# Kernel tuning notes

Hardware: AMD Instinct MI355X
Metric: run time of the kernel (lower is better)

## Reference

```python
import jax, jax.numpy as jnp
from jax import lax
import numpy as np

B, CIN, H, W = 64, 3, 256, 256
K, D = 512, 4
EPS = 1e-5

def conv(x, w, s, p):
    return lax.conv_general_dilated(x, w, (s, s), [(p, p), (p, p)],
                                    dimension_numbers=('NCHW', 'OIHW', 'NCHW'))

def convT(x, w, s, p):
    # w in torch ConvTranspose2d layout (Cin, Cout, kh, kw)
    wt = jnp.flip(w, (2, 3)).transpose(1, 0, 2, 3)
    kh, kw = w.shape[2], w.shape[3]
    pad = [(kh - 1 - p, kh - 1 - p), (kw - 1 - p, kw - 1 - p)]
    return lax.conv_general_dilated(x, wt, (1, 1), pad, lhs_dilation=(s, s),
                                    dimension_numbers=('NCHW', 'OIHW', 'NCHW'))

def bn(x, g, b):
    # training-mode BatchNorm2d: batch stats over (N,H,W), biased variance
    m = jnp.mean(x, (0, 2, 3), keepdims=True)
    v = jnp.var(x, (0, 2, 3), keepdims=True)
    return g[None, :, None, None] * (x - m) * lax.rsqrt(v + EPS) + b[None, :, None, None]

def setup_inputs() -> dict:
    key = jax.random.key(0)
    ks = jax.random.split(key, 8)
    rn = lambda k, s: jax.random.normal(k, s, jnp.float32) * 0.05
    return {
        'x': jax.random.uniform(ks[0], (B, CIN, H, W), jnp.float32),
        'enc_w1': rn(ks[1], (8, CIN, 5, 5)),
        'enc_g1': jnp.ones(8, jnp.float32), 'enc_b1': jnp.zeros(8, jnp.float32),
        'enc_w2': rn(ks[2], (16, 8, 3, 3)),
        'enc_g2': jnp.ones(16, jnp.float32), 'enc_b2': jnp.zeros(16, jnp.float32),
        'enc_w3': rn(ks[3], (D, 16, 3, 3)),
        'enc_g3': jnp.ones(D, jnp.float32), 'enc_b3': jnp.zeros(D, jnp.float32),
        'emb': jax.random.uniform(ks[4], (K, D), jnp.float32, -1.0 / K, 1.0 / K),
        'dec_w1': rn(ks[5], (D, 16, 3, 3)),
        'dec_g1': jnp.ones(16, jnp.float32), 'dec_b1': jnp.zeros(16, jnp.float32),
        'dec_w2': rn(ks[6], (16, 8, 3, 3)),
        'dec_g2': jnp.ones(8, jnp.float32), 'dec_b2': jnp.zeros(8, jnp.float32),
        'dec_w3': rn(ks[7], (8, CIN, 2, 2)),
        'dec_bias3': jnp.zeros(CIN, jnp.float32),
    }

def reference(x, enc_w1, enc_g1, enc_b1, enc_w2, enc_g2, enc_b2,
              enc_w3, enc_g3, enc_b3, emb,
              dec_w1, dec_g1, dec_b1, dec_w2, dec_g2, dec_b2,
              dec_w3, dec_bias3):
    # encoder: 256 -> 127 -> 64 -> 32
    h1 = jax.nn.relu(bn(conv(x, enc_w1, 2, 1), enc_g1, enc_b1))
    h2 = jax.nn.relu(bn(conv(h1, enc_w2, 2, 1), enc_g2, enc_b2))
    latents = jax.nn.relu(bn(conv(h2, enc_w3, 2, 1), enc_g3, enc_b3))  # [B, D, h, w]
    Bq, Dq, h, w = latents.shape
    z = latents.transpose(0, 2, 3, 1).reshape(-1, Dq)  # [N, D] tokens
    # VQ: squared L2 distances (expanded form, as in 'efficient' path), argmin, gather
    dist = (jnp.sum(z * z, 1, keepdims=True)
            - 2.0 * (z @ emb.T)
            + jnp.sum(emb * emb, 1)[None, :])  # [N, K]
    closest = jnp.argmin(dist, axis=-1)
    codes = emb[closest]  # same math as one-hot @ emb
    codebook_loss = jnp.mean((codes - lax.stop_gradient(z)) ** 2)
    commitment_loss = jnp.mean((lax.stop_gradient(codes) - z) ** 2)
    codes = z + lax.stop_gradient(codes - z)  # straight-through
    quantized = codes.reshape(Bq, h, w, Dq).transpose(0, 3, 1, 2)  # [B, D, h, w]
    # decoder: 32 -> 65 -> 129 -> 256
    g1 = jax.nn.relu(bn(convT(quantized, dec_w1, 2, 0), dec_g1, dec_b1))
    g2 = jax.nn.relu(bn(convT(g1, dec_w2, 2, 1), dec_g2, dec_b2))
    decoded = jax.nn.sigmoid(convT(g2, dec_w3, 2, 1) + dec_bias3[None, :, None, None])
    return (latents, quantized, decoded, codebook_loss, commitment_loss)
```

## Files before the change

kernel.cpp:

```cpp
#include <hip/hip_runtime.h>
#include <hip/hip_bf16.h>
#include <math.h>


#define EPSV 1e-5f

template<int CIN, int COUT, int KH, int KW, int S, int P,
         int IH, int IW, int OH, int OW, bool FUSE>
__global__ __launch_bounds__(256)
void conv_all(const float* __restrict__ in, const float* __restrict__ w,
              const float* __restrict__ ssin, float* __restrict__ out,
              float* __restrict__ psum, float* __restrict__ psq) {
    __shared__ float wl[COUT * CIN * KH * KW];
    __shared__ float ssl[2 * CIN];
    __shared__ float redbuf[4 * 2 * COUT];
    const int n = blockIdx.z;
    for (int i = threadIdx.x; i < COUT * CIN * KH * KW; i += 256) wl[i] = w[i];
    if constexpr (FUSE) {
        for (int i = threadIdx.x; i < 2 * CIN; i += 256) ssl[i] = ssin[i];
    }
    __syncthreads();

    const int p = blockIdx.x * 256 + threadIdx.x;
    const int oy = p / OW, ox = p % OW;
    float acc[COUT];
    #pragma unroll
    for (int co = 0; co < COUT; ++co) acc[co] = 0.f;

    if (p < OH * OW) {
        const int iy0 = oy * S - P, ix0 = ox * S - P;
        const float* inb = in + (size_t)n * CIN * IH * IW;
        #pragma unroll
        for (int ci = 0; ci < CIN; ++ci) {
            #pragma unroll
            for (int kh = 0; kh < KH; ++kh) {
                const int iy = iy0 + kh;
                if ((unsigned)iy < (unsigned)IH) {
                    #pragma unroll
                    for (int kw = 0; kw < KW; ++kw) {
                        const int ix = ix0 + kw;
                        if ((unsigned)ix < (unsigned)IW) {
                            float v = inb[(ci * IH + iy) * IW + ix];
                            if constexpr (FUSE)
                                v = fmaxf(v * ssl[2 * ci] + ssl[2 * ci + 1], 0.f);
                            #pragma unroll
                            for (int co = 0; co < COUT; ++co)
                                acc[co] += v * wl[((co * CIN + ci) * KH + kh) * KW + kw];
                        }
                    }
                }
            }
        }
        #pragma unroll
        for (int co = 0; co < COUT; ++co)
            out[(((size_t)n * COUT + co) * OH + oy) * OW + ox] = acc[co];
    }

    const int lane = threadIdx.x & 63, wid = threadIdx.x >> 6;
    #pragma unroll
    for (int co = 0; co < COUT; ++co) {
        float s = acc[co], q = acc[co] * acc[co];
        #pragma unroll
        for (int o = 32; o > 0; o >>= 1) {
            s += __shfl_down(s, o, 64);
            q += __shfl_down(q, o, 64);
        }
        if (lane == 0) {
            redbuf[wid * 2 * COUT + 2 * co]     = s;
            redbuf[wid * 2 * COUT + 2 * co + 1] = q;
        }
    }
    __syncthreads();
    if (threadIdx.x < 2 * COUT) {
        const float v = redbuf[threadIdx.x] + redbuf[2 * COUT + threadIdx.x]
                      + redbuf[4 * COUT + threadIdx.x] + redbuf[6 * COUT + threadIdx.x];
        const int co = threadIdx.x >> 1;
        const int bid = blockIdx.z * gridDim.x + blockIdx.x;
        const int NB  = gridDim.x * gridDim.z;
        if (threadIdx.x & 1) psq[co * NB + bid] = v;
        else                 psum[co * NB + bid] = v;
    }
}

template<int CIN, int COUT, int KH, int KW, int P,
         int IH, int IW, int OH, int OW, bool FUSE>
__global__ __launch_bounds__(256)
void convT_all(const float* __restrict__ in, const float* __restrict__ w,
               const float* __restrict__ ssin, float* __restrict__ out,
               float* __restrict__ psum, float* __restrict__ psq) {
    __shared__ float wl[CIN * COUT * KH * KW];
    __shared__ float ssl[2 * CIN];
    __shared__ float redbuf[4 * 2 * COUT];
    const int n = blockIdx.z;
    for (int i = threadIdx.x; i < CIN * COUT * KH * KW; i += 256) wl[i] = w[i];
    if constexpr (FUSE) {
        for (int i = threadIdx.x; i < 2 * CIN; i += 256) ssl[i] = ssin[i];
    }
    __syncthreads();

    const int p = blockIdx.x * 256 + threadIdx.x;
    const int oy = p / OW, ox = p % OW;
    float acc[COUT];
    #pragma unroll
    for (int co = 0; co < COUT; ++co) acc[co] = 0.f;

    if (p < OH * OW) {
        const float* inb = in + (size_t)n * CIN * IH * IW;
        #pragma unroll
        for (int kh = 0; kh < KH; ++kh) {
            const int t = oy + P - kh;
            const int iy = t >> 1;
            if (t >= 0 && (t & 1) == 0 && iy < IH) {
                #pragma unroll
                for (int kw = 0; kw < KW; ++kw) {
                    const int u = ox + P - kw;
                    const int ix = u >> 1;
                    if (u >= 0 && (u & 1) == 0 && ix < IW) {
                        #pragma unroll
                        for (int ci = 0; ci < CIN; ++ci) {
                            float v = inb[(ci * IH + iy) * IW + ix];
                            if constexpr (FUSE)
                                v = fmaxf(v * ssl[2 * ci] + ssl[2 * ci + 1], 0.f);
                            #pragma unroll
                            for (int co = 0; co < COUT; ++co)
                                acc[co] += v * wl[((ci * COUT + co) * KH + kh) * KW + kw];
                        }
                    }
                }
            }
        }
        #pragma unroll
        for (int co = 0; co < COUT; ++co)
            out[(((size_t)n * COUT + co) * OH + oy) * OW + ox] = acc[co];
    }

    const int lane = threadIdx.x & 63, wid = threadIdx.x >> 6;
    #pragma unroll
    for (int co = 0; co < COUT; ++co) {
        float s = acc[co], q = acc[co] * acc[co];
        #pragma unroll
        for (int o = 32; o > 0; o >>= 1) {
            s += __shfl_down(s, o, 64);
            q += __shfl_down(q, o, 64);
        }
        if (lane == 0) {
            redbuf[wid * 2 * COUT + 2 * co]     = s;
            redbuf[wid * 2 * COUT + 2 * co + 1] = q;
        }
    }
    __syncthreads();
    if (threadIdx.x < 2 * COUT) {
        const float v = redbuf[threadIdx.x] + redbuf[2 * COUT + threadIdx.x]
                      + redbuf[4 * COUT + threadIdx.x] + redbuf[6 * COUT + threadIdx.x];
        const int co = threadIdx.x >> 1;
        const int bid = blockIdx.z * gridDim.x + blockIdx.x;
        const int NB  = gridDim.x * gridDim.z;
        if (threadIdx.x & 1) psq[co * NB + bid] = v;
        else                 psum[co * NB + bid] = v;
    }
}

template<int C>
__global__ __launch_bounds__(64)
void red_final_k(const float* __restrict__ psum, const float* __restrict__ psq,
                 const float* __restrict__ g, const float* __restrict__ b,
                 float* __restrict__ ss, float inv_count, int NB) {
    const int c = blockIdx.x;
    float s = 0.f, q = 0.f;
    for (int i = threadIdx.x; i < NB; i += 64) { s += psum[c * NB + i]; q += psq[c * NB + i]; }
    #pragma unroll
    for (int o = 32; o > 0; o >>= 1) {
        s += __shfl_down(s, o, 64);
        q += __shfl_down(q, o, 64);
    }
    if (threadIdx.x == 0) {
        const float mean = s * inv_count;
        const float var  = q * inv_count - mean * mean;
        const float rstd = 1.f / sqrtf(var + EPSV);
        const float sc   = g[c] * rstd;
        ss[2 * c]     = sc;
        ss[2 * c + 1] = b[c] - mean * sc;
    }
}

__global__ __launch_bounds__(256)
void vq_k(const float* __restrict__ raw, const float* __restrict__ ss,
          const float* __restrict__ emb, float* __restrict__ out_lat,
          float* __restrict__ out_q, float* __restrict__ lossp) {
    __shared__ float e[512 * 4];
    __shared__ float ee[512];
    __shared__ float ssl[8];
    __shared__ float redbuf[4];
    for (int i = threadIdx.x; i < 512 * 4; i += 256) e[i] = emb[i];
    if (threadIdx.x < 8) ssl[threadIdx.x] = ss[threadIdx.x];
    __syncthreads();
    for (int k = threadIdx.x; k < 512; k += 256) {
        float s = 0.f;
        #pragma unroll
        for (int d = 0; d < 4; ++d) { const float v = e[k * 4 + d]; s += v * v; }
        ee[k] = s;
    }
    __syncthreads();

    const int t = blockIdx.x * 256 + threadIdx.x;
    const int b = t >> 10, p = t & 1023;
    const float* rb = raw + ((size_t)b * 4) * 1024 + p;
    const float z0 = fmaxf(rb[0]    * ssl[0] + ssl[1], 0.f);
    const float z1 = fmaxf(rb[1024] * ssl[2] + ssl[3], 0.f);
    const float z2 = fmaxf(rb[2048] * ssl[4] + ssl[5], 0.f);
    const float z3 = fmaxf(rb[3072] * ssl[6] + ssl[7], 0.f);
    float* lb = out_lat + ((size_t)b * 4) * 1024 + p;
    lb[0] = z0; lb[1024] = z1; lb[2048] = z2; lb[3072] = z3;

    const float zz = z0 * z0 + z1 * z1 + z2 * z2 + z3 * z3;
    int best = 0;
    float bd = INFINITY;
    #pragma unroll 8
    for (int k = 0; k < 512; ++k) {
        const float dot = z0 * e[k * 4] + z1 * e[k * 4 + 1] + z2 * e[k * 4 + 2] + z3 * e[k * 4 + 3];
        const float d = zz - 2.f * dot + ee[k];
        if (d < bd) { bd = d; best = k; }
    }
    const float q0 = e[best * 4], q1 = e[best * 4 + 1], q2 = e[best * 4 + 2], q3 = e[best * 4 + 3];
    float* qb = out_q + ((size_t)b * 4) * 1024 + p;
    qb[0] = q0; qb[1024] = q1; qb[2048] = q2; qb[3072] = q3;

    float ssd = (q0 - z0) * (q0 - z0) + (q1 - z1) * (q1 - z1)
              + (q2 - z2) * (q2 - z2) + (q3 - z3) * (q3 - z3);
    #pragma unroll
    for (int o = 32; o > 0; o >>= 1) ssd += __shfl_down(ssd, o, 64);
    const int lane = threadIdx.x & 63, wid = threadIdx.x >> 6;
    if (lane == 0) redbuf[wid] = ssd;
    __syncthreads();
    if (threadIdx.x == 0)
        lossp[blockIdx.x] = redbuf[0] + redbuf[1] + redbuf[2] + redbuf[3];
}

__global__ __launch_bounds__(256)
void loss_final_k(const float* __restrict__ partial, float* __restrict__ out_cb,
                  float* __restrict__ out_cm) {
    __shared__ float redbuf[4];
    float s = partial[threadIdx.x];
    #pragma unroll
    for (int o = 32; o > 0; o >>= 1) s += __shfl_down(s, o, 64);
    const int lane = threadIdx.x & 63, wid = threadIdx.x >> 6;
    if (lane == 0) redbuf[wid] = s;
    __syncthreads();
    if (threadIdx.x == 0) {
        const float L = (redbuf[0] + redbuf[1] + redbuf[2] + redbuf[3]) * (1.f / 262144.f);
        *out_cb = L;
        *out_cm = L;
    }
}

__global__ __launch_bounds__(256)
void convt3_k(const float* __restrict__ in, const float* __restrict__ w,
              const float* __restrict__ ss, const float* __restrict__ bias,
              float* __restrict__ out) {
    __shared__ float wl[8 * 3 * 4];
    __shared__ float ssl[16];
    __shared__ float bl[3];
    if (threadIdx.x < 96) wl[threadIdx.x] = w[threadIdx.x];
    if (threadIdx.x < 16) ssl[threadIdx.x] = ss[threadIdx.x];
    if (threadIdx.x < 3)  bl[threadIdx.x] = bias[threadIdx.x];
    __syncthreads();

    const int n = blockIdx.z;
    const int p = blockIdx.x * 256 + threadIdx.x;
    const int oy = p >> 8, ox = p & 255;
    const int kh = 1 - (oy & 1), kw = 1 - (ox & 1);
    const int iy = (oy + 1 - kh) >> 1, ix = (ox + 1 - kw) >> 1;
    const float* inb = in + (size_t)n * 8 * 129 * 129;

    float a0 = bl[0], a1 = bl[1], a2 = bl[2];
    const int wo = kh * 2 + kw;
    #pragma unroll
    for (int ci = 0; ci < 8; ++ci) {
        float v = inb[(ci * 129 + iy) * 129 + ix];
        v = fmaxf(v * ssl[2 * ci] + ssl[2 * ci + 1], 0.f);
        a0 += v * wl[(ci * 3 + 0) * 4 + wo];
        a1 += v * wl[(ci * 3 + 1) * 4 + wo];
        a2 += v * wl[(ci * 3 + 2) * 4 + wo];
    }
    a0 = 1.f / (1.f + expf(-a0));
    a1 = 1.f / (1.f + expf(-a1));
    a2 = 1.f / (1.f + expf(-a2));
    float* ob = out + ((size_t)n * 3 * 65536) + (size_t)oy * 256 + ox;
    ob[0] = a0; ob[65536] = a1; ob[131072] = a2;
}

extern "C" void kernel_launch(void* const* d_in, const int* in_sizes, int n_in,
                              void* d_out, int out_size, void* d_ws, size_t ws_size,
                              hipStream_t stream) {
    const float* x      = (const float*)d_in[0];
    const float* ew1    = (const float*)d_in[1];
    const float* eg1    = (const float*)d_in[2];
    const float* eb1    = (const float*)d_in[3];
    const float* ew2    = (const float*)d_in[4];
    const float* eg2    = (const float*)d_in[5];
    const float* eb2    = (const float*)d_in[6];
    const float* ew3    = (const float*)d_in[7];
    const float* eg3    = (const float*)d_in[8];
    const float* eb3    = (const float*)d_in[9];
    const float* emb    = (const float*)d_in[10];
    const float* dw1    = (const float*)d_in[11];
    const float* dg1    = (const float*)d_in[12];
    const float* db1    = (const float*)d_in[13];
    const float* dw2    = (const float*)d_in[14];
    const float* dg2    = (const float*)d_in[15];
    const float* db2    = (const float*)d_in[16];
    const float* dw3    = (const float*)d_in[17];
    const float* dbias3 = (const float*)d_in[18];

    float* out_lat = (float*)d_out;
    float* out_q   = out_lat + 262144;
    float* out_dec = out_q + 262144;
    float* out_cb  = (float*)d_out + 13107200;
    float* out_cm  = out_cb + 1;

    float* bufA  = (float*)d_ws;
    float* bufB  = bufA + 8520768;
    float* bufC  = bufB + 4326400;
    float* psum  = bufC + 262144;
    float* psq   = psum + 33792;
    float* ssb   = psq + 33792;
    float* lossp = ssb + 32;

    const int T = 256;

    conv_all<3, 8, 5, 5, 2, 1, 256, 256, 127, 127, false>
        <<<dim3(64, 1, 64), T, 0, stream>>>(x, ew1, nullptr, bufA, psum, psq);
    red_final_k<8><<<8, 64, 0, stream>>>(psum, psq, eg1, eb1, ssb,
                                         1.f / (64.f * 16129.f), 64 * 64);

    conv_all<8, 16, 3, 3, 2, 1, 127, 127, 64, 64, true>
        <<<dim3(16, 1, 64), T, 0, stream>>>(bufA, ew2, ssb, bufB, psum, psq);
    red_final_k<16><<<16, 64, 0, stream>>>(psum, psq, eg2, eb2, ssb,
                                           1.f / (64.f * 4096.f), 16 * 64);

    conv_all<16, 4, 3, 3, 2, 1, 64, 64, 32, 32, true>
        <<<dim3(4, 1, 64), T, 0, stream>>>(bufB, ew3, ssb, bufC, psum, psq);
    red_final_k<4><<<4, 64, 0, stream>>>(psum, psq, eg3, eb3, ssb,
                                         1.f / (64.f * 1024.f), 4 * 64);

    vq_k<<<256, T, 0, stream>>>(bufC, ssb, emb, out_lat, out_q, lossp);
    loss_final_k<<<1, T, 0, stream>>>(lossp, out_cb, out_cm);

    convT_all<4, 16, 3, 3, 0, 32, 32, 65, 65, false>
        <<<dim3(17, 1, 64), T, 0, stream>>>(out_q, dw1, nullptr, bufB, psum, psq);
    red_final_k<16><<<16, 64, 0, stream>>>(psum, psq, dg1, db1, ssb,
                                           1.f / (64.f * 4225.f), 17 * 64);

    convT_all<16, 8, 3, 3, 1, 65, 65, 129, 129, true>
        <<<dim3(66, 1, 64), T, 0, stream>>>(bufB, dw2, ssb, bufA, psum, psq);
    red_final_k<8><<<8, 64, 0, stream>>>(psum, psq, dg2, db2, ssb,
                                         1.f / (64.f * 16641.f), 66 * 64);

    convt3_k<<<dim3(256, 1, 64), T, 0, stream>>>(bufA, dw3, ssb, dbias3, out_dec);
}
```

Measured before the change: 504.8 us.

## Replace generic conv kernels with specialized per-layer tiled and parity-split kernels

Replaces the generic templated conv and transposed-conv kernels with a hand-specialized kernel per layer. The first conv stages an input tile in shared memory and computes several outputs per thread. The transposed convs are split by output-row parity so that only the valid taps are evaluated instead of branching on stride residues. The last decoder layer computes 2x2 outputs per thread and writes them as float2 with fast exp. The goals are more register reuse of weights, fewer wasted taps and better coalescing, at the cost of much more layer-specific code and index logic that must be checked for correctness.

```diff
diff --git a/kernel.cpp b/kernel.cpp
--- a/kernel.cpp
+++ b/kernel.cpp
@@ -5,158 +5,31 @@
 
 #define EPSV 1e-5f
 
-template<int CIN, int COUT, int KH, int KW, int S, int P,
-         int IH, int IW, int OH, int OW, bool FUSE>
-__global__ __launch_bounds__(256)
-void conv_all(const float* __restrict__ in, const float* __restrict__ w,
-              const float* __restrict__ ssin, float* __restrict__ out,
-              float* __restrict__ psum, float* __restrict__ psq) {
-    __shared__ float wl[COUT * CIN * KH * KW];
-    __shared__ float ssl[2 * CIN];
-    __shared__ float redbuf[4 * 2 * COUT];
-    const int n = blockIdx.z;
-    for (int i = threadIdx.x; i < COUT * CIN * KH * KW; i += 256) wl[i] = w[i];
-    if constexpr (FUSE) {
-        for (int i = threadIdx.x; i < 2 * CIN; i += 256) ssl[i] = ssin[i];
-    }
-    __syncthreads();
-
-    const int p = blockIdx.x * 256 + threadIdx.x;
-    const int oy = p / OW, ox = p % OW;
-    float acc[COUT];
-    #pragma unroll
-    for (int co = 0; co < COUT; ++co) acc[co] = 0.f;
-
-    if (p < OH * OW) {
-        const int iy0 = oy * S - P, ix0 = ox * S - P;
-        const float* inb = in + (size_t)n * CIN * IH * IW;
-        #pragma unroll
-        for (int ci = 0; ci < CIN; ++ci) {
-            #pragma unroll
-            for (int kh = 0; kh < KH; ++kh) {
-                const int iy = iy0 + kh;
-                if ((unsigned)iy < (unsigned)IH) {
-                    #pragma unroll
-                    for (int kw = 0; kw < KW; ++kw) {
-                        const int ix = ix0 + kw;
-                        if ((unsigned)ix < (unsigned)IW) {
-                            float v = inb[(ci * IH + iy) * IW + ix];
-                            if constexpr (FUSE)
-                                v = fmaxf(v * ssl[2 * ci] + ssl[2 * ci + 1], 0.f);
-                            #pragma unroll
-                            for (int co = 0; co < COUT; ++co)
-                                acc[co] += v * wl[((co * CIN + ci) * KH + kh) * KW + kw];
-                        }
-                    }
-                }
-            }
-        }
-        #pragma unroll
-        for (int co = 0; co < COUT; ++co)
-            out[(((size_t)n * COUT + co) * OH + oy) * OW + ox] = acc[co];
-    }
-
-    const int lane = threadIdx.x & 63, wid = threadIdx.x >> 6;
+template<int COUT, int NW>
+__device__ __forceinline__ void stats_write(float (&s)[COUT], float (&q)[COUT],
+    float* __restrict__ psum, float* __restrict__ psq, int bid, int NB,
+    float* redbuf, int tid) {
+    const int lane = tid & 63, wid = tid >> 6;
     #pragma unroll
     for (int co = 0; co < COUT; ++co) {
-        float s = acc[co], q = acc[co] * acc[co];
+        float ss = s[co], qq = q[co];
         #pragma unroll
         for (int o = 32; o > 0; o >>= 1) {
-            s += __shfl_down(s, o, 64);
-            q += __shfl_down(q, o, 64);
+            ss += __shfl_down(ss, o, 64);
+            qq += __shfl_down(qq, o, 64);
         }
         if (lane == 0) {
-            redbuf[wid * 2 * COUT + 2 * co]     = s;
-            redbuf[wid * 2 * COUT + 2 * co + 1] = q;
-        }
-    }
-    __syncthreads();
-    if (threadIdx.x < 2 * COUT) {
-        const float v = redbuf[threadIdx.x] + redbuf[2 * COUT + threadIdx.x]
-                      + redbuf[4 * COUT + threadIdx.x] + redbuf[6 * COUT + threadIdx.x];
-        const int co = threadIdx.x >> 1;
-        const int bid = blockIdx.z * gridDim.x + blockIdx.x;
-        const int NB  = gridDim.x * gridDim.z;
-        if (threadIdx.x & 1) psq[co * NB + bid] = v;
-        else                 psum[co * NB + bid] = v;
-    }
-}
-
-template<int CIN, int COUT, int KH, int KW, int P,
-         int IH, int IW, int OH, int OW, bool FUSE>
-__global__ __launch_bounds__(256)
-void convT_all(const float* __restrict__ in, const float* __restrict__ w,
-               const float* __restrict__ ssin, float* __restrict__ out,
-               float* __restrict__ psum, float* __restrict__ psq) {
-    __shared__ float wl[CIN * COUT * KH * KW];
-    __shared__ float ssl[2 * CIN];
-    __shared__ float redbuf[4 * 2 * COUT];
-    const int n = blockIdx.z;
-    for (int i = threadIdx.x; i < CIN * COUT * KH * KW; i += 256) wl[i] = w[i];
-    if constexpr (FUSE) {
-        for (int i = threadIdx.x; i < 2 * CIN; i += 256) ssl[i] = ssin[i];
-    }
-    __syncthreads();
-
-    const int p = blockIdx.x * 256 + threadIdx.x;
-    const int oy = p / OW, ox = p % OW;
-    float acc[COUT];
-    #pragma unroll
-    for (int co = 0; co < COUT; ++co) acc[co] = 0.f;
-
-    if (p < OH * OW) {
-        const float* inb = in + (size_t)n * CIN * IH * IW;
-        #pragma unroll
-        for (int kh = 0; kh < KH; ++kh) {
-            const int t = oy + P - kh;
-            const int iy = t >> 1;
-            if (t >= 0 && (t & 1) == 0 && iy < IH) {
-                #pragma unroll
-                for (int kw = 0; kw < KW; ++kw) {
-                    const int u = ox + P - kw;
-                    const int ix = u >> 1;
-                    if (u >= 0 && (u & 1) == 0 && ix < IW) {
-                        #pragma unroll
-                        for (int ci = 0; ci < CIN; ++ci) {
-                            float v = inb[(ci * IH + iy) * IW + ix];
-                            if constexpr (FUSE)
-                                v = fmaxf(v * ssl[2 * ci] + ssl[2 * ci + 1], 0.f);
-                            #pragma unroll
-                            for (int co = 0; co < COUT; ++co)
-                                acc[co] += v * wl[((ci * COUT + co) * KH + kh) * KW + kw];
-                        }
-                    }
-                }
-            }
-        }
-        #pragma unroll
-        for (int co = 0; co < COUT; ++co)
-            out[(((size_t)n * COUT + co) * OH + oy) * OW + ox] = acc[co];
-    }
-
-    const int lane = threadIdx.x & 63, wid = threadIdx.x >> 6;
-    #pragma unroll
-    for (int co = 0; co < COUT; ++co) {
-        float s = acc[co], q = acc[co] * acc[co];
-        #pragma unroll
-        for (int o = 32; o > 0; o >>= 1) {
-            s += __shfl_down(s, o, 64);
-            q += __shfl_down(q, o, 64);
-        }
-        if (lane == 0) {
-            redbuf[wid * 2 * COUT + 2 * co]     = s;
-            redbuf[wid * 2 * COUT + 2 * co + 1] = q;
-        }
-    }
-    __syncthreads();
-    if (threadIdx.x < 2 * COUT) {
-        const float v = redbuf[threadIdx.x] + redbuf[2 * COUT + threadIdx.x]
-                      + redbuf[4 * COUT + threadIdx.x] + redbuf[6 * COUT + threadIdx.x];
-        const int co = threadIdx.x >> 1;
-        const int bid = blockIdx.z * gridDim.x + blockIdx.x;
-        const int NB  = gridDim.x * gridDim.z;
-        if (threadIdx.x & 1) psq[co * NB + bid] = v;
-        else                 psum[co * NB + bid] = v;
+            redbuf[wid * 2 * COUT + 2 * co]     = ss;
+            redbuf[wid * 2 * COUT + 2 * co + 1] = qq;
+        }
+    }
+    __syncthreads();
+    if (tid < 2 * COUT) {
+        float v = 0.f;
+        #pragma unroll
+        for (int w = 0; w < NW; ++w) v += redbuf[w * 2 * COUT + tid];
+        if (tid & 1) psq [(tid >> 1) * NB + bid] = v;
+        else         psum[(tid >> 1) * NB + bid] = v;
     }
 }
 
@@ -181,6 +54,208 @@
         ss[2 * c]     = sc;
         ss[2 * c + 1] = b[c] - mean * sc;
     }
+}
+
+__global__ __launch_bounds__(128)
+void conv1_k(const float* __restrict__ in, const float* __restrict__ w,
+             float* __restrict__ out, float* __restrict__ psum,
+             float* __restrict__ psq) {
+    __shared__ float tile[3 * 11 * 264];
+    __shared__ float wl[600];
+    __shared__ float redbuf[2 * 2 * 8];
+    const int tid = threadIdx.x;
+    const int by = blockIdx.y, n = blockIdx.z;
+
+    for (int i = tid; i < 600; i += 128) {
+        const int co = i & 7, rest = i >> 3;
+        wl[i] = w[co * 75 + rest];
+    }
+    const int iy_org = 8 * by - 1;
+    const float* inb = in + (size_t)n * 3 * 256 * 256;
+    for (int i = tid; i < 3 * 11 * 264; i += 128) {
+        const int c = i % 264, rc = i / 264, r = rc % 11, ci = rc / 11;
+        const int gy = iy_org + r, gx = c - 1;
+        float v = 0.f;
+        if (c < 258 && (unsigned)gy < 256u && (unsigned)gx < 256u)
+            v = inb[(ci * 256 + gy) * 256 + gx];
+        tile[(ci * 11 + r) * 264 + c] = v;
+    }
+    __syncthreads();
+
+    const int ty = tid >> 5, tx = tid & 31;
+    const int oy = 4 * by + ty;
+    float acc[4][8];
+    #pragma unroll
+    for (int p = 0; p < 4; ++p)
+        #pragma unroll
+        for (int co = 0; co < 8; ++co) acc[p][co] = 0.f;
+
+    #pragma unroll
+    for (int ci = 0; ci < 3; ++ci) {
+        #pragma unroll
+        for (int kh = 0; kh < 5; ++kh) {
+            const float* trow = &tile[(ci * 11 + 2 * ty + kh) * 264];
+            #pragma unroll
+            for (int kw = 0; kw < 5; ++kw) {
+                float wv[8];
+                #pragma unroll
+                for (int co = 0; co < 8; ++co)
+                    wv[co] = wl[((ci * 5 + kh) * 5 + kw) * 8 + co];
+                #pragma unroll
+                for (int p = 0; p < 4; ++p) {
+                    const float v = trow[2 * (tx + 32 * p) + kw];
+                    #pragma unroll
+                    for (int co = 0; co < 8; ++co) acc[p][co] = fmaf(v, wv[co], acc[p][co]);
+                }
+            }
+        }
+    }
+    if (oy >= 127) {
+        #pragma unroll
+        for (int p = 0; p < 4; ++p)
+            #pragma unroll
+            for (int co = 0; co < 8; ++co) acc[p][co] = 0.f;
+    }
+    #pragma unroll
+    for (int p = 0; p < 4; ++p)
+        if (tx + 32 * p >= 127) {
+            #pragma unroll
+            for (int co = 0; co < 8; ++co) acc[p][co] = 0.f;
+        }
+    if (oy < 127) {
+        #pragma unroll
+        for (int p = 0; p < 4; ++p) {
+            const int ox = tx + 32 * p;
+            if (ox < 127) {
+                #pragma unroll
+                for (int co = 0; co < 8; ++co)
+                    out[(((size_t)n * 8 + co) * 127 + oy) * 127 + ox] = acc[p][co];
+            }
+        }
+    }
+    float s[8], q[8];
+    #pragma unroll
+    for (int co = 0; co < 8; ++co) {
+        s[co] = acc[0][co] + acc[1][co] + acc[2][co] + acc[3][co];
+        q[co] = acc[0][co] * acc[0][co] + acc[1][co] * acc[1][co]
+              + acc[2][co] * acc[2][co] + acc[3][co] * acc[3][co];
+    }
+    stats_write<8, 2>(s, q, psum, psq, n * 32 + by, 2048, redbuf, tid);
+}
+
+__global__ __launch_bounds__(256)
+void conv2_k(const float* __restrict__ in, const float* __restrict__ w,
+             const float* __restrict__ ssin, float* __restrict__ out,
+             float* __restrict__ psum, float* __restrict__ psq) {
+    __shared__ float wl[8 * 9 * 16];
+    __shared__ float ssl[16];
+    __shared__ float redbuf[4 * 2 * 16];
+    const int tid = threadIdx.x;
+    const int by = blockIdx.y, n = blockIdx.z;
+    for (int i = tid; i < 1152; i += 256) {
+        const int co = i & 15, rest = i >> 4;
+        wl[i] = w[co * 72 + rest];
+    }
+    if (tid < 16) ssl[tid] = ssin[tid];
+    __syncthreads();
+
+    const int ty = tid >> 5, tx = tid & 31;
+    const int oy = 8 * by + ty;
+    const float* inb = in + (size_t)n * 8 * 127 * 127;
+    float acc[2][16];
+    #pragma unroll
+    for (int p = 0; p < 2; ++p)
+        #pragma unroll
+        for (int co = 0; co < 16; ++co) acc[p][co] = 0.f;
+
+    #pragma unroll
+    for (int ci = 0; ci < 8; ++ci) {
+        const float sc = ssl[2 * ci], sh = ssl[2 * ci + 1];
+        #pragma unroll
+        for (int kh = 0; kh < 3; ++kh) {
+            const int iy = 2 * oy - 1 + kh;
+            const bool vy = (unsigned)iy < 127u;
+            #pragma unroll
+            for (int kw = 0; kw < 3; ++kw) {
+                float wv[16];
+                #pragma unroll
+                for (int co = 0; co < 16; ++co)
+                    wv[co] = wl[(ci * 9 + kh * 3 + kw) * 16 + co];
+                #pragma unroll
+                for (int p = 0; p < 2; ++p) {
+                    const int ox = tx + 32 * p;
+                    const int ix = 2 * ox - 1 + kw;
+                    float v = 0.f;
+                    if (vy && (unsigned)ix < 127u)
+                        v = fmaxf(inb[(ci * 127 + iy) * 127 + ix] * sc + sh, 0.f);
+                    #pragma unroll
+                    for (int co = 0; co < 16; ++co) acc[p][co] = fmaf(v, wv[co], acc[p][co]);
+                }
+            }
+        }
+    }
+    #pragma unroll
+    for (int p = 0; p < 2; ++p) {
+        const int ox = tx + 32 * p;
+        #pragma unroll
+        for (int co = 0; co < 16; ++co)
+            out[(((size_t)n * 16 + co) * 64 + oy) * 64 + ox] = acc[p][co];
+    }
+    float s[16], q[16];
+    #pragma unroll
+    for (int co = 0; co < 16; ++co) {
+        s[co] = acc[0][co] + acc[1][co];
+        q[co] = acc[0][co] * acc[0][co] + acc[1][co] * acc[1][co];
+    }
+    stats_write<16, 4>(s, q, psum, psq, n * 8 + by, 512, redbuf, tid);
+}
+
+__global__ __launch_bounds__(256)
+void conv3_k(const float* __restrict__ in, const float* __restrict__ w,
+             const float* __restrict__ ssin, float* __restrict__ out,
+             float* __restrict__ psum, float* __restrict__ psq) {
+    __shared__ float wl[16 * 9 * 4];
+    __shared__ float ssl[32];
+    __shared__ float redbuf[4 * 2 * 4];
+    const int tid = threadIdx.x;
+    const int bx = blockIdx.x, n = blockIdx.z;
+    for (int i = tid; i < 576; i += 256) {
+        const int co = i & 3, rest = i >> 2;
+        wl[i] = w[co * 144 + rest];
+    }
+    if (tid < 32) ssl[tid] = ssin[tid];
+    __syncthreads();
+
+    const int p = bx * 256 + tid;
+    const int oy = p >> 5, ox = p & 31;
+    const float* inb = in + (size_t)n * 16 * 64 * 64;
+    float acc[4] = {0.f, 0.f, 0.f, 0.f};
+    #pragma unroll
+    for (int ci = 0; ci < 16; ++ci) {
+        const float sc = ssl[2 * ci], sh = ssl[2 * ci + 1];
+        #pragma unroll
+        for (int kh = 0; kh < 3; ++kh) {
+            const int iy = 2 * oy - 1 + kh;
+            const bool vy = (unsigned)iy < 64u;
+            #pragma unroll
+            for (int kw = 0; kw < 3; ++kw) {
+                const int ix = 2 * ox - 1 + kw;
+                float v = 0.f;
+                if (vy && (unsigned)ix < 64u)
+                    v = fmaxf(inb[(ci * 64 + iy) * 64 + ix] * sc + sh, 0.f);
+                #pragma unroll
+                for (int co = 0; co < 4; ++co)
+                    acc[co] = fmaf(v, wl[(ci * 9 + kh * 3 + kw) * 4 + co], acc[co]);
+            }
+        }
+    }
+    #pragma unroll
+    for (int co = 0; co < 4; ++co)
+        out[((size_t)n * 4 + co) * 1024 + p] = acc[co];
+    float s[4], q[4];
+    #pragma unroll
+    for (int co = 0; co < 4; ++co) { s[co] = acc[co]; q[co] = acc[co] * acc[co]; }
+    stats_write<4, 4>(s, q, psum, psq, n * 4 + bx, 256, redbuf, tid);
 }
 
 __global__ __launch_bounds__(256)
@@ -254,39 +329,185 @@
 }
 
 __global__ __launch_bounds__(256)
-void convt3_k(const float* __restrict__ in, const float* __restrict__ w,
-              const float* __restrict__ ss, const float* __restrict__ bias,
-              float* __restrict__ out) {
-    __shared__ float wl[8 * 3 * 4];
+void dect1_k(const float* __restrict__ in, const float* __restrict__ w,
+             float* __restrict__ out, float* __restrict__ psum,
+             float* __restrict__ psq) {
+    __shared__ float wl[4 * 9 * 16];
+    __shared__ float redbuf[4 * 2 * 16];
+    const int tid = threadIdx.x;
+    const int cy = blockIdx.y, n = blockIdx.z;
+    for (int i = tid; i < 576; i += 256) {
+        const int co = i & 15, rest = i >> 4;
+        const int ci = rest / 9, k = rest % 9;
+        wl[i] = w[(ci * 16 + co) * 9 + k];
+    }
+    __syncthreads();
+
+    const int Ry = 33 - cy;
+    const int p = blockIdx.x * 256 + tid;
+    const bool active = p < Ry * 33;
+    const int ry = p / 33, rx = p % 33;
+    const int oy = 2 * ry + cy;
+    float acc_e[16], acc_o[16];
+    #pragma unroll
+    for (int co = 0; co < 16; ++co) { acc_e[co] = 0.f; acc_o[co] = 0.f; }
+
+    if (active) {
+        const float* inb = in + (size_t)n * 4 * 1024;
+        auto tap = [&](int kh, int iy, bool vy) {
+            #pragma unroll
+            for (int ci = 0; ci < 4; ++ci) {
+                const float* r = inb + (ci * 32 + iy) * 32;
+                const float vL = (vy && rx >= 1) ? r[rx - 1] : 0.f;
+                const float vR = (vy && rx < 32) ? r[rx]     : 0.f;
+                const float* wp = &wl[(ci * 9 + kh * 3) * 16];
+                #pragma unroll
+                for (int co = 0; co < 16; ++co) {
+                    acc_e[co] = fmaf(vR, wp[co], fmaf(vL, wp[32 + co], acc_e[co]));
+                    acc_o[co] = fmaf(vR, wp[16 + co], acc_o[co]);
+                }
+            }
+        };
+        if (cy == 0) { tap(0, ry, ry < 32); tap(2, ry - 1, ry >= 1); }
+        else         { tap(1, ry, true); }
+
+        #pragma unroll
+        for (int co = 0; co < 16; ++co) {
+            float* o = out + (((size_t)n * 16 + co) * 65 + oy) * 65 + 2 * rx;
+            o[0] = acc_e[co];
+            if (rx < 32) o[1] = acc_o[co];
+        }
+    }
+    float s[16], q[16];
+    #pragma unroll
+    for (int co = 0; co < 16; ++co) {
+        s[co] = acc_e[co] + acc_o[co];
+        q[co] = acc_e[co] * acc_e[co] + acc_o[co] * acc_o[co];
+    }
+    stats_write<16, 4>(s, q, psum, psq, (n * 2 + cy) * 5 + blockIdx.x, 640, redbuf, tid);
+}
+
+__global__ __launch_bounds__(256)
+void dect2_k(const float* __restrict__ in, const float* __restrict__ w,
+             const float* __restrict__ ssin, float* __restrict__ out,
+             float* __restrict__ psum, float* __restrict__ psq) {
+    __shared__ float wl[16 * 9 * 8];
+    __shared__ float ssl[32];
+    __shared__ float redbuf[4 * 2 * 8];
+    const int tid = threadIdx.x;
+    const int cy = blockIdx.y, n = blockIdx.z;
+    for (int i = tid; i < 1152; i += 256) {
+        const int co = i & 7, rest = i >> 3;
+        const int ci = rest / 9, k = rest % 9;
+        wl[i] = w[(ci * 8 + co) * 9 + k];
+    }
+    if (tid < 32) ssl[tid] = ssin[tid];
+    __syncthreads();
+
+    const int Ry = 65 - cy;
+    const int p = blockIdx.x * 256 + tid;
+    const bool active = p < Ry * 65;
+    const int ry = p / 65, rx = p % 65;
+    const int oy = 2 * ry + cy;
+    float acc_e[8], acc_o[8];
+    #pragma unroll
+    for (int co = 0; co < 8; ++co) { acc_e[co] = 0.f; acc_o[co] = 0.f; }
+
+    if (active) {
+        const float* inb = in + (size_t)n * 16 * 65 * 65;
+        auto tap = [&](int kh, int iy) {
+            #pragma unroll
+            for (int ci = 0; ci < 16; ++ci) {
+                const float sc = ssl[2 * ci], sh = ssl[2 * ci + 1];
+                const float* r = inb + (ci * 65 + iy) * 65;
+                const float vR = fmaxf(r[rx] * sc + sh, 0.f);
+                float vP = 0.f;
+                if (rx < 64) vP = fmaxf(r[rx + 1] * sc + sh, 0.f);
+                const float* wp = &wl[(ci * 9 + kh * 3) * 8];
+                #pragma unroll
+                for (int co = 0; co < 8; ++co) {
+                    acc_e[co] = fmaf(vR, wp[8 + co], acc_e[co]);
+                    acc_o[co] = fmaf(vP, wp[co], fmaf(vR, wp[16 + co], acc_o[co]));
+                }
+            }
+        };
+        if (cy == 0) { tap(1, ry); }
+        else         { tap(0, ry + 1); tap(2, ry); }
+
+        if (rx >= 64) {
+            #pragma unroll
+            for (int co = 0; co < 8; ++co) acc_o[co] = 0.f;
+        }
+        #pragma unroll
+        for (int co = 0; co < 8; ++co) {
+            float* o = out + (((size_t)n * 8 + co) * 129 + oy) * 129 + 2 * rx;
+            o[0] = acc_e[co];
+            if (rx < 64) o[1] = acc_o[co];
+        }
+    }
+    float s[8], q[8];
+    #pragma unroll
+    for (int co = 0; co < 8; ++co) {
+        s[co] = acc_e[co] + acc_o[co];
+        q[co] = acc_e[co] * acc_e[co] + acc_o[co] * acc_o[co];
+    }
+    stats_write<8, 4>(s, q, psum, psq, (n * 2 + cy) * 17 + blockIdx.x, 2176, redbuf, tid);
+}
+
+__global__ __launch_bounds__(256)
+void dec3_k(const float* __restrict__ in, const float* __restrict__ w,
+            const float* __restrict__ ssin, const float* __restrict__ bias,
+            float* __restrict__ out) {
+    __shared__ float wl[96];
     __shared__ float ssl[16];
     __shared__ float bl[3];
-    if (threadIdx.x < 96) wl[threadIdx.x] = w[threadIdx.x];
-    if (threadIdx.x < 16) ssl[threadIdx.x] = ss[threadIdx.x];
-    if (threadIdx.x < 3)  bl[threadIdx.x] = bias[threadIdx.x];
+    const int tid = threadIdx.x;
+    if (tid < 96) wl[tid] = w[tid];
+    if (tid < 16) ssl[tid] = ssin[tid];
+    if (tid < 3)  bl[tid] = bias[tid];
     __syncthreads();
 
     const int n = blockIdx.z;
-    const int p = blockIdx.x * 256 + threadIdx.x;
-    const int oy = p >> 8, ox = p & 255;
-    const int kh = 1 - (oy & 1), kw = 1 - (ox & 1);
-    const int iy = (oy + 1 - kh) >> 1, ix = (ox + 1 - kw) >> 1;
+    const int p = blockIdx.x * 256 + tid;
+    const int ry = p >> 7, rx = p & 127;
     const float* inb = in + (size_t)n * 8 * 129 * 129;
 
-    float a0 = bl[0], a1 = bl[1], a2 = bl[2];
-    const int wo = kh * 2 + kw;
+    float acc[2][2][3];
+    #pragma unroll
+    for (int dy = 0; dy < 2; ++dy)
+        #pragma unroll
+        for (int dx = 0; dx < 2; ++dx)
+            #pragma unroll
+            for (int co = 0; co < 3; ++co) acc[dy][dx][co] = bl[co];
+
     #pragma unroll
     for (int ci = 0; ci < 8; ++ci) {
-        float v = inb[(ci * 129 + iy) * 129 + ix];
-        v = fmaxf(v * ssl[2 * ci] + ssl[2 * ci + 1], 0.f);
-        a0 += v * wl[(ci * 3 + 0) * 4 + wo];
-        a1 += v * wl[(ci * 3 + 1) * 4 + wo];
-        a2 += v * wl[(ci * 3 + 2) * 4 + wo];
-    }
-    a0 = 1.f / (1.f + expf(-a0));
-    a1 = 1.f / (1.f + expf(-a1));
-    a2 = 1.f / (1.f + expf(-a2));
-    float* ob = out + ((size_t)n * 3 * 65536) + (size_t)oy * 256 + ox;
-    ob[0] = a0; ob[65536] = a1; ob[131072] = a2;
+        const float sc = ssl[2 * ci], sh = ssl[2 * ci + 1];
+        const float* base = inb + (ci * 129 + ry) * 129 + rx;
+        const float v00 = fmaxf(base[0]   * sc + sh, 0.f);
+        const float v01 = fmaxf(base[1]   * sc + sh, 0.f);
+        const float v10 = fmaxf(base[129] * sc + sh, 0.f);
+        const float v11 = fmaxf(base[130] * sc + sh, 0.f);
+        #pragma unroll
+        for (int co = 0; co < 3; ++co) {
+            const int b = (ci * 3 + co) * 4;
+            acc[0][0][co] = fmaf(v00, wl[b + 3], acc[0][0][co]);
+            acc[0][1][co] = fmaf(v01, wl[b + 2], acc[0][1][co]);
+            acc[1][0][co] = fmaf(v10, wl[b + 1], acc[1][0][co]);
+            acc[1][1][co] = fmaf(v11, wl[b + 0], acc[1][1][co]);
+        }
+    }
+    #pragma unroll
+    for (int co = 0; co < 3; ++co) {
+        #pragma unroll
+        for (int dy = 0; dy < 2; ++dy) {
+            float a0 = 1.f / (1.f + __expf(-acc[dy][0][co]));
+            float a1 = 1.f / (1.f + __expf(-acc[dy][1][co]));
+            float2 v2 = make_float2(a0, a1);
+            float* o = out + (((size_t)n * 3 + co) << 16) + (size_t)(2 * ry + dy) * 256 + 2 * rx;
+            *reinterpret_cast<float2*>(o) = v2;
+        }
+    }
 }
 
 extern "C" void kernel_launch(void* const* d_in, const int* in_sizes, int n_in,
@@ -322,39 +543,26 @@
     float* bufB  = bufA + 8520768;
     float* bufC  = bufB + 4326400;
     float* psum  = bufC + 262144;
-    float* psq   = psum + 33792;
-    float* ssb   = psq + 33792;
+    float* psq   = psum + 18432;
+    float* ssb   = psq + 18432;
     float* lossp = ssb + 32;
 
-    const int T = 256;
-
-    conv_all<3, 8, 5, 5, 2, 1, 256, 256, 127, 127, false>
-        <<<dim3(64, 1, 64), T, 0, stream>>>(x, ew1, nullptr, bufA, psum, psq);
+    conv1_k<<<dim3(1, 32, 64), 128, 0, stream>>>(x, ew1, bufA, psum, psq);
     red_final_k<8><<<8, 64, 0, stream>>>(psum, psq, eg1, eb1, ssb,
-                                         1.f / (64.f * 16129.f), 64 * 64);
-
-    conv_all<8, 16, 3, 3, 2, 1, 127, 127, 64, 64, true>
-        <<<dim3(16, 1, 64), T, 0, stream>>>(bufA, ew2, ssb, bufB, psum, psq);
+                                         1.f / (64.f * 16129.f), 2048);
+    conv2_k<<<dim3(1, 8, 64), 256, 0, stream>>>(bufA, ew2, ssb, bufB, psum, psq);
     red_final_k<16><<<16, 64, 0, stream>>>(psum, psq, eg2, eb2, ssb,
-                                           1.f / (64.f * 4096.f), 16 * 64);
-
-    conv_all<16, 4, 3, 3, 2, 1, 64, 64, 32, 32, true>
-        <<<dim3(4, 1, 64), T, 0, stream>>>(bufB, ew3, ssb, bufC, psum, psq);
+                                           1.f / (64.f * 4096.f), 512);
+    conv3_k<<<dim3(4, 1, 64), 256, 0, stream>>>(bufB, ew3, ssb, bufC, psum, psq);
     red_final_k<4><<<4, 64, 0, stream>>>(psum, psq, eg3, eb3, ssb,
-                                         1.f / (64.f * 1024.f), 4 * 64);
-
-    vq_k<<<256, T, 0, stream>>>(bufC, ssb, emb, out_lat, out_q, lossp);
-    loss_final_k<<<1, T, 0, stream>>>(lossp, out_cb, out_cm);
-
-    convT_all<4, 16, 3, 3, 0, 32, 32, 65, 65, false>
-        <<<dim3(17, 1, 64), T, 0, stream>>>(out_q, dw1, nullptr, bufB, psum, psq);
+                                         1.f / (64.f * 1024.f), 256);
+    vq_k<<<256, 256, 0, stream>>>(bufC, ssb, emb, out_lat, out_q, lossp);
+    loss_final_k<<<1, 256, 0, stream>>>(lossp, out_cb, out_cm);
+    dect1_k<<<dim3(5, 2, 64), 256, 0, stream>>>(out_q, dw1, bufB, psum, psq);
     red_final_k<16><<<16, 64, 0, stream>>>(psum, psq, dg1, db1, ssb,
-                                           1.f / (64.f * 4225.f), 17 * 64);
-
-    convT_all<16, 8, 3, 3, 1, 65, 65, 129, 129, true>
-        <<<dim3(66, 1, 64), T, 0, stream>>>(bufB, dw2, ssb, bufA, psum, psq);
+                                           1.f / (64.f * 4225.f), 640);
+    dect2_k<<<dim3(17, 2, 64), 256, 0, stream>>>(bufB, dw2, ssb, bufA, psum, psq);
     red_final_k<8><<<8, 64, 0, stream>>>(psum, psq, dg2, db2, ssb,
-                                         1.f / (64.f * 16641.f), 66 * 64);
-
-    convt3_k<<<dim3(256, 1, 64), T, 0, stream>>>(bufA, dw3, ssb, dbias3, out_dec);
-}
+                                         1.f / (64.f * 16641.f), 2176);
+    dec3_k<<<dim3(64, 1, 64), 256, 0, stream>>>(bufA, dw3, ssb, dbias3, out_dec);
+}
```

New measurement: 1.143 ms. 126% more time.
